# Kernel optimization log

Hardware: AMD Instinct MI355X
Metric: run time of the kernel (lower is better)

## Reference

```python
import jax, jax.numpy as jnp
import numpy as np

B, H, W = 4, 256, 256
IN_HSI, IN_MSI, EMBED = 31, 3, 128
R = 2
MAX_FLOW = 2.0
REG_IN = EMBED + EMBED + (2 * R + 1) ** 2 + 1  # 282


def _conv(x, w, b=None, pad=0, groups=1):
    out = jax.lax.conv_general_dilated(
        x, w, (1, 1), [(pad, pad), (pad, pad)],
        dimension_numbers=('NCHW', 'OIHW', 'NCHW'), feature_group_count=groups)
    if b is not None:
        out = out + b[None, :, None, None]
    return out


def _gauss_window(size=9, sigma=1.5):
    c = jnp.arange(size, dtype=jnp.float32) - (size - 1) / 2.0
    g = jnp.exp(-(c ** 2) / (2.0 * sigma ** 2))
    g = g / g.sum()
    return g[:, None] * g[None, :]


def _ssim_map(a, b, win=9):
    # standard gaussian-window SSIM, per-pixel map averaged over channels
    C = a.shape[1]
    w2d = _gauss_window(win)
    k = jnp.broadcast_to(w2d[None, None], (C, 1, win, win))
    pad = win // 2
    dw = lambda t: _conv(t, k, pad=pad, groups=C)
    mu1, mu2 = dw(a), dw(b)
    mu1s, mu2s, mu12 = mu1 * mu1, mu2 * mu2, mu1 * mu2
    s1 = dw(a * a) - mu1s
    s2 = dw(b * b) - mu2s
    s12 = dw(a * b) - mu12
    C1, C2 = 0.01 ** 2, 0.03 ** 2
    m = ((2 * mu12 + C1) * (2 * s12 + C2)) / ((mu1s + mu2s + C1) * (s1 + s2 + C2))
    return m.mean(axis=1)  # (B,H,W)


def _match_mean_std(src, ref, eps=1e-6):
    sm = src.mean(axis=(2, 3), keepdims=True)
    ss = src.std(axis=(2, 3), keepdims=True, ddof=1)  # torch std is unbiased
    rm = ref.mean(axis=(2, 3), keepdims=True)
    rs = ref.std(axis=(2, 3), keepdims=True, ddof=1)
    return (src - sm) / (ss + eps) * rs + rm


def _l2norm(t, eps=1e-12):
    n = jnp.sqrt(jnp.sum(t * t, axis=1, keepdims=True))
    return t / jnp.maximum(n, eps)


def _corr_volume(q, k, r=R):
    _, _, h, w = q.shape
    q = _l2norm(q)
    k = _l2norm(k)
    kp = jnp.pad(k, ((0, 0), (0, 0), (r, r), (r, r)), mode='edge')  # replicate pad
    outs = []
    for dy in range(-r, r + 1):
        for dx in range(-r, r + 1):
            ks = kp[:, :, r + dy:r + dy + h, r + dx:r + dx + w]
            outs.append(jnp.sum(q * ks, axis=1))
    return jnp.stack(outs, axis=1)  # (B, 25, H, W)


def _reflect(coord, size):
    # PyTorch grid_sample reflection, align_corners=False: reflect about -0.5 and size-0.5
    min_ = -0.5
    span = float(size)
    c = jnp.abs(coord - min_)
    extra = jnp.mod(c, span)
    flips = jnp.floor(c / span)
    c = jnp.where(jnp.mod(flips, 2.0) == 0.0, extra + min_, span - extra + min_)
    return jnp.clip(c, 0.0, size - 1.0)


def _warp(img, flow):
    b, c, h, w = img.shape
    gx = (-1.0 + (2.0 * jnp.arange(w, dtype=img.dtype) + 1.0) / w)[None, None, :] + flow[:, 0] * (2.0 / w)
    gy = (-1.0 + (2.0 * jnp.arange(h, dtype=img.dtype) + 1.0) / h)[None, :, None] + flow[:, 1] * (2.0 / h)
    ix = _reflect(((gx + 1.0) * w - 1.0) / 2.0, w)
    iy = _reflect(((gy + 1.0) * h - 1.0) / 2.0, h)
    x0 = jnp.floor(ix)
    y0 = jnp.floor(iy)
    wx = ix - x0
    wy = iy - y0
    x0i = jnp.clip(x0.astype(jnp.int32), 0, w - 1)
    x1i = jnp.clip(x0i + 1, 0, w - 1)
    y0i = jnp.clip(y0.astype(jnp.int32), 0, h - 1)
    y1i = jnp.clip(y0i + 1, 0, h - 1)
    bi = jnp.arange(b)[:, None, None]
    g = lambda yi, xi: img[bi, :, yi, xi]  # (B,H,W,C)
    out = (g(y0i, x0i) * ((1 - wy) * (1 - wx))[..., None]
           + g(y0i, x1i) * ((1 - wy) * wx)[..., None]
           + g(y1i, x0i) * (wy * (1 - wx))[..., None]
           + g(y1i, x1i) * (wy * wx)[..., None])
    return jnp.transpose(out, (0, 3, 1, 2))


def setup_inputs() -> dict:
    key = jax.random.key(0)
    ks = jax.random.split(key, 16)

    def rn(k, shape, fan_in):
        return (jax.random.normal(k, shape, dtype=jnp.float32) / np.sqrt(fan_in)).astype(jnp.float32)

    return {
        'x': jax.random.normal(ks[0], (B, 2 * IN_HSI, H, W), dtype=jnp.float32),
        'y': jax.random.normal(ks[1], (B, IN_MSI, H, W), dtype=jnp.float32),
        'SRF': jax.random.uniform(ks[2], (IN_MSI, IN_HSI), dtype=jnp.float32) / IN_HSI,
        'conv_half_w': rn(ks[3], (IN_HSI, 2 * IN_HSI, 1, 1), 2 * IN_HSI),
        'conv_half_b': jnp.zeros((IN_HSI,), jnp.float32),
        'q_w': rn(ks[4], (EMBED, IN_HSI, 1, 1), IN_HSI),
        'q_b': jnp.zeros((EMBED,), jnp.float32),
        'k_w': rn(ks[5], (EMBED, IN_MSI, 1, 1), IN_MSI),
        'k_b': jnp.zeros((EMBED,), jnp.float32),
        'r1_w': rn(ks[6], (128, REG_IN, 3, 3), REG_IN * 9),
        'r1_b': jnp.zeros((128,), jnp.float32),
        'r2_w': rn(ks[7], (64, 128, 3, 3), 128 * 9),
        'r2_b': jnp.zeros((64,), jnp.float32),
        'r3_w': rn(ks[8], (2, 64, 1, 1), 64) * 0.1,
        'r3_b': jnp.zeros((2,), jnp.float32),
    }


def reference(x, y, SRF, conv_half_w, conv_half_b, q_w, q_b, k_w, k_b,
              r1_w, r1_b, r2_w, r2_b, r3_w, r3_b):
    x = _conv(x, conv_half_w, conv_half_b)
    x_original = x
    srf_w = SRF[:, :, None, None]  # (in_msi, in_hsi, 1, 1)
    x_projected = jnp.clip(_conv(x, srf_w), -1.0, 1.0)
    x_aligned = jnp.clip(_match_mean_std(x_projected, y), -1.0, 1.0)
    ssim_score = _ssim_map(x_aligned, y, 9)
    difficulty = jnp.clip((1.0 - ssim_score)[:, None] / 2.0, 0.0, 1.0)  # (B,1,H,W)
    q = _conv(x, q_w, q_b)
    k = _conv(y, k_w, k_b)
    corr = _corr_volume(q, k, R)
    reg_in = jnp.concatenate([q, k, corr, difficulty], axis=1)
    h1 = jax.nn.leaky_relu(_conv(reg_in, r1_w, r1_b, pad=1), 0.2)
    h2 = jax.nn.leaky_relu(_conv(h1, r2_w, r2_b, pad=1), 0.2)
    flow = jnp.tanh(_conv(h2, r3_w, r3_b)) * MAX_FLOW * difficulty
    return _warp(x_original, flow)
```

## Files before the change

### kernel.cpp

```cpp
#include <hip/hip_runtime.h>
#include <hip/hip_bf16.h>
#include <math.h>


#define HH 256
#define WWI 256
#define HW 65536
#define CH 31
#define CIN2 62
#define CM 3
#define CE 128
#define REGC 288
#define C1S 1e-4f
#define C2S 9e-4f

typedef unsigned short u16;
typedef unsigned int u32;
typedef short bf16x8 __attribute__((ext_vector_type(8)));
typedef float f32x4 __attribute__((ext_vector_type(4)));

__device__ __forceinline__ float blo(u32 u){ return __uint_as_float(u << 16); }
__device__ __forceinline__ float bhi(u32 u){ return __uint_as_float(u & 0xffff0000u); }
__device__ __forceinline__ float b1f(u16 u){ return __uint_as_float(((u32)u) << 16); }
__device__ __forceinline__ u16 f2b(float f){
    u32 u = __float_as_uint(f);
    u32 r = (u + 0x7fffu + ((u >> 16) & 1u)) >> 16;
    return (u16)r;
}
__device__ __forceinline__ f32x4 mfma16(bf16x8 a, bf16x8 b, f32x4 c){
    return __builtin_amdgcn_mfma_f32_16x16x32_bf16(a, b, c, 0, 0, 0);
}

__global__ void k_conv_half(const float* __restrict__ x, const float* __restrict__ w,
                            const float* __restrict__ bias, u16* __restrict__ x31){
    __shared__ float sw[CH*CIN2];
    __shared__ float sb[CH+1];
    for(int i=threadIdx.x;i<CH*CIN2;i+=256) sw[i]=w[i];
    for(int i=threadIdx.x;i<CH;i+=256) sb[i]=bias[i];
    __syncthreads();
    int pixg = blockIdx.x*256 + threadIdx.x;
    int b = pixg>>16, hw = pixg&65535;
    float acc[CH];
    #pragma unroll
    for(int c=0;c<CH;c++) acc[c]=sb[c];
    for(int ci=0;ci<CIN2;ci++){
        float xv = x[((size_t)(b*CIN2+ci))*HW + hw];
        #pragma unroll
        for(int c=0;c<CH;c++) acc[c] += sw[c*CIN2+ci]*xv;
    }
    u16* o = x31 + (size_t)pixg*32;
    #pragma unroll
    for(int c=0;c<CH;c++) o[c]=f2b(acc[c]);
    o[31]=0;
}

__global__ void k_project(const u16* __restrict__ x31, const float* __restrict__ srf,
                          float* __restrict__ xp){
    __shared__ float s[CM*CH];
    for(int i=threadIdx.x;i<CM*CH;i+=256) s[i]=srf[i];
    __syncthreads();
    int pixg = blockIdx.x*256 + threadIdx.x;
    int b = pixg>>16, hw = pixg&65535;
    const u16* xr = x31 + (size_t)pixg*32;
    float xv[CH];
    #pragma unroll
    for(int c=0;c<CH;c++) xv[c] = b1f(xr[c]);
    #pragma unroll
    for(int m=0;m<CM;m++){
        float acc=0.f;
        #pragma unroll
        for(int c=0;c<CH;c++) acc += s[m*CH+c]*xv[c];
        acc = fminf(fmaxf(acc,-1.f),1.f);
        xp[((size_t)(b*CM+m))*HW + hw] = acc;
    }
}

__global__ void k_stats1(const float* __restrict__ xp, const float* __restrict__ y,
                         float2* __restrict__ part, int NB){
    int bid = blockIdx.x;
    int p = bid >> 6, c = bid & 63;
    const float* src = (p<3*NB) ? (xp + (size_t)p*HW) : (y + (size_t)(p-3*NB)*HW);
    const float4* s4 = (const float4*)(src + c*1024);
    float4 v = s4[threadIdx.x];
    float s  = v.x + v.y + v.z + v.w;
    float ss = v.x*v.x + v.y*v.y + v.z*v.z + v.w*v.w;
    #pragma unroll
    for(int t=1;t<64;t<<=1){ s += __shfl_xor(s,t); ss += __shfl_xor(ss,t); }
    __shared__ float rs[4], rss[4];
    int wid = threadIdx.x>>6, lane = threadIdx.x&63;
    if(lane==0){ rs[wid]=s; rss[wid]=ss; }
    __syncthreads();
    if(threadIdx.x==0){
        part[bid] = float2{rs[0]+rs[1]+rs[2]+rs[3], rss[0]+rss[1]+rss[2]+rss[3]};
    }
}

__global__ void k_stats2(const float2* __restrict__ part, float* __restrict__ stats){
    int p = blockIdx.x;
    float2 pa = part[p*64 + threadIdx.x];
    float s = pa.x, ss = pa.y;
    #pragma unroll
    for(int t=1;t<64;t<<=1){ s += __shfl_xor(s,t); ss += __shfl_xor(ss,t); }
    if(threadIdx.x==0){
        float mean = s/(float)HW;
        float var = (ss - s*s/(float)HW) / (float)(HW-1);
        stats[p*2]   = mean;
        stats[p*2+1] = sqrtf(fmaxf(var,0.f));
    }
}

__global__ __launch_bounds__(256) void k_ssim(const float* __restrict__ xp,
                                              const float* __restrict__ y,
                                              const float* __restrict__ stats,
                                              float* __restrict__ diff,
                                              u16* __restrict__ regin, int NB){
    __shared__ float sxa[1600];
    __shared__ float sy2[1600];
    __shared__ float hs[5][1280];
    int t = threadIdx.x;
    int bid = blockIdx.x;
    int bb = bid >> 6;
    int s2 = bid & 63;
    int tx = s2 & 7, ty = s2 >> 3;
    float g[9]; float gs = 0.f;
    #pragma unroll
    for(int k=0;k<9;k++){ float cc=(float)(k-4); g[k]=expf(-cc*cc/4.5f); gs+=g[k]; }
    float ginv = 1.f/gs;
    #pragma unroll
    for(int k=0;k<9;k++) g[k] *= ginv;

    float msum[4] = {0.f,0.f,0.f,0.f};
    for(int m=0;m<3;m++){
        int plane = bb*3+m;
        float sm = stats[plane*2],        ssd = stats[plane*2+1];
        float rm = stats[(plane+3*NB)*2], rsd = stats[(plane+3*NB)*2+1];
        const float* xpp = xp + (size_t)plane*HW;
        const float* yp  = y  + (size_t)plane*HW;
        if(m) __syncthreads();
        #pragma unroll
        for(int it=0; it<7; ++it){
            int s = it*256 + t;
            if(s < 1600){
                int rr = s/40, cc = s - rr*40;
                int gy = ty*32-4+rr, gx = tx*32-4+cc;
                float xv=0.f, yv=0.f;
                if(((unsigned)gy<256u)&&((unsigned)gx<256u)){
                    float v = xpp[(gy<<8)+gx];
                    v = (v-sm)/(ssd+1e-6f)*rsd + rm;
                    xv = fminf(fmaxf(v,-1.f),1.f);
                    yv = yp[(gy<<8)+gx];
                }
                sxa[s]=xv; sy2[s]=yv;
            }
        }
        __syncthreads();
        #pragma unroll
        for(int it=0; it<5; ++it){
            int s = it*256 + t;
            int rr = s>>5, cc = s&31;
            int base = rr*40 + cc;
            float s0=0,s1=0,s2v=0,s3=0,s4=0;
            #pragma unroll
            for(int k=0;k<9;k++){
                float gg=g[k];
                float a=sxa[base+k], b=sy2[base+k];
                s0+=gg*a; s1+=gg*b; s2v+=gg*a*a; s3+=gg*b*b; s4+=gg*a*b;
            }
            hs[0][s]=s0; hs[1][s]=s1; hs[2][s]=s2v; hs[3][s]=s3; hs[4][s]=s4;
        }
        __syncthreads();
        #pragma unroll
        for(int it=0; it<4; ++it){
            int s = it*256 + t;
            int rr = s>>5, cc = s&31;
            float v0=0,v1=0,v2=0,v3=0,v4=0;
            #pragma unroll
            for(int k=0;k<9;k++){
                float gg=g[k];
                int idx=(rr+k)*32+cc;
                v0+=gg*hs[0][idx]; v1+=gg*hs[1][idx]; v2+=gg*hs[2][idx];
                v3+=gg*hs[3][idx]; v4+=gg*hs[4][idx];
            }
            float mu1=v0, mu2=v1;
            float mu1s=mu1*mu1, mu2s=mu2*mu2, mu12=mu1*mu2;
            float sg1=v2-mu1s, sg2=v3-mu2s, sg12=v4-mu12;
            msum[it] += (2.f*mu12+C1S)*(2.f*sg12+C2S)
                      / ((mu1s+mu2s+C1S)*(sg1+sg2+C2S));
        }
    }
    #pragma unroll
    for(int it=0; it<4; ++it){
        int s = it*256 + t;
        int rr = s>>5, cc = s&31;
        int pixg = (bb<<16) + ((ty*32+rr)<<8) + (tx*32+cc);
        float d = fminf(fmaxf((1.f-msum[it]*(1.f/3.f))*0.5f,0.f),1.f);
        diff[pixg] = d;
        regin[(size_t)pixg*REGC + 281] = f2b(d);
    }
}

__global__ __launch_bounds__(128) void k_qk(const u16* __restrict__ x31,
                     const float* __restrict__ y,
                     const float* __restrict__ qw, const float* __restrict__ qb,
                     const float* __restrict__ kw, const float* __restrict__ kb,
                     u16* __restrict__ regin){
    __shared__ float sqw[CE*CH];
    __shared__ float skw[CE*CM];
    __shared__ float sqb[CE], skb[CE];
    for(int i=threadIdx.x;i<CE*CH;i+=128) sqw[i]=qw[i];
    for(int i=threadIdx.x;i<CE*CM;i+=128) skw[i]=kw[i];
    if(threadIdx.x<CE){ sqb[threadIdx.x]=qb[threadIdx.x]; skb[threadIdx.x]=kb[threadIdx.x]; }
    __syncthreads();
    int co = threadIdx.x;
    int p0 = blockIdx.x*32;
    float wk0 = skw[co*CM+0], wk1 = skw[co*CM+1], wk2 = skw[co*CM+2];
    for(int pp=0;pp<32;pp++){
        int pixg = p0+pp;
        int b = pixg>>16, hw = pixg&65535;
        const u16* xr = x31 + (size_t)pixg*32;
        float acc = sqb[co];
        #pragma unroll
        for(int c=0;c<CH;c++) acc += sqw[co*CH+c]*b1f(xr[c]);
        u16* rg = regin + (size_t)pixg*REGC;
        rg[co] = f2b(acc);
        float ack = skb[co] + wk0*y[((size_t)(b*CM  ))*HW+hw]
                            + wk1*y[((size_t)(b*CM+1))*HW+hw]
                            + wk2*y[((size_t)(b*CM+2))*HW+hw];
        rg[128+co] = f2b(ack);
        if(co<6) rg[282+co] = 0;
    }
}

__global__ __launch_bounds__(256) void k_corr(const u16* __restrict__ regin,
                                              u16* __restrict__ regout){
    __shared__ uint4 klv[288*16];
    __shared__ float kinvl[288];
    int t = threadIdx.x;
    int half = t & 1, pidx = t >> 1;
    int bid = blockIdx.x;
    int bb = bid >> 9;
    int s2 = bid & 511;
    int tx = s2 & 7, ty = s2 >> 3;
    int lw = pidx & 31, lh = pidx >> 5;
    int w = tx*32 + lw;
    int h = ty*4 + lh;
    int pixg = (bb<<16) + (h<<8) + w;

    #pragma unroll
    for(int it=0; it<18; ++it){
        int s = it*256 + t;
        int rpx = s >> 4, g = s & 15;
        int rr = rpx/36, cc = rpx - rr*36;
        int gy = min(max(ty*4-2+rr,0),255);
        int gx = min(max(tx*32-2+cc,0),255);
        const uint4* src = (const uint4*)(regin + ((size_t)((bb<<16)+(gy<<8)+gx))*REGC + 128);
        klv[rpx*16 + (g ^ (rpx&15))] = src[g];
    }
    __syncthreads();

    #pragma unroll
    for(int it=0; it<3; ++it){
        int item = it*256 + t;
        int px = item>>1, hf = item&1;
        float s = 0.f;
        if(item < 576){
            const uint4* kp = &klv[px*16];
            int sw = px & 15;
            #pragma unroll
            for(int i=0;i<8;i++){
                uint4 kv = kp[(hf*8+i)^sw];
                s += blo(kv.x)*blo(kv.x)+bhi(kv.x)*bhi(kv.x)
                   + blo(kv.y)*blo(kv.y)+bhi(kv.y)*bhi(kv.y)
                   + blo(kv.z)*blo(kv.z)+bhi(kv.z)*bhi(kv.z)
                   + blo(kv.w)*blo(kv.w)+bhi(kv.w)*bhi(kv.w);
            }
        }
        float so = s + __shfl_xor(s,1);
        if(item < 576 && hf==0) kinvl[px] = 1.f/fmaxf(sqrtf(so),1e-12f);
    }
    __syncthreads();

    uint4 q[8];
    const uint4* qp = (const uint4*)(regin + (size_t)pixg*REGC) + half*8;
    #pragma unroll
    for(int i=0;i<8;i++) q[i] = qp[i];
    float sq = 0.f;
    #pragma unroll
    for(int i=0;i<8;i++){
        uint4 v = q[i];
        sq += blo(v.x)*blo(v.x)+bhi(v.x)*bhi(v.x) + blo(v.y)*blo(v.y)+bhi(v.y)*bhi(v.y)
            + blo(v.z)*blo(v.z)+bhi(v.z)*bhi(v.z) + blo(v.w)*blo(v.w)+bhi(v.w)*bhi(v.w);
    }
    sq += __shfl_xor(sq, 1);
    float qn = 1.f/fmaxf(sqrtf(sq),1e-12f);

    float res[13];
    #pragma unroll
    for(int dy=-2;dy<=2;dy++){
        #pragma unroll
        for(int dx=-2;dx<=2;dx++){
            int rpx = (lh+2+dy)*36 + (lw+2+dx);
            const uint4* kp = &klv[rpx*16];
            int sw = rpx & 15;
            float s = 0.f;
            #pragma unroll
            for(int i=0;i<8;i++){
                uint4 kv = kp[(half*8 + i) ^ sw];
                uint4 qv = q[i];
                s += blo(qv.x)*blo(kv.x) + bhi(qv.x)*bhi(kv.x);
                s += blo(qv.y)*blo(kv.y) + bhi(qv.y)*bhi(kv.y);
                s += blo(qv.z)*blo(kv.z) + bhi(qv.z)*bhi(kv.z);
                s += blo(qv.w)*blo(kv.w) + bhi(qv.w)*bhi(kv.w);
            }
            s += __shfl_xor(s, 1);
            float cv = s*qn*kinvl[rpx];
            int o = (dy+2)*5 + (dx+2);
            if(o < 13){ if(half==0) res[o] = cv; }
            else      { if(half==1) res[o-13] = cv; }
        }
    }

    u16* rg = regout + (size_t)pixg*REGC + 256;
    if(half==0){
        u16 p[13];
        #pragma unroll
        for(int i=0;i<13;i++) p[i] = f2b(res[i]);
        uint4 v0; u32* v0p = (u32*)&v0;
        #pragma unroll
        for(int i=0;i<4;i++) v0p[i] = (u32)p[2*i] | ((u32)p[2*i+1]<<16);
        *(uint4*)(rg) = v0;
        *(u32*)(rg+8)  = (u32)p[8]  | ((u32)p[9]<<16);
        *(u32*)(rg+10) = (u32)p[10] | ((u32)p[11]<<16);
        rg[12] = p[12];
    } else {
        u16 p[12];
        #pragma unroll
        for(int i=0;i<12;i++) p[i] = f2b(res[i]);
        rg[13] = p[0];
        *(u32*)(rg+14) = (u32)p[1] | ((u32)p[2]<<16);
        uint4 v1; u32* v1p = (u32*)&v1;
        #pragma unroll
        for(int i=0;i<4;i++) v1p[i] = (u32)p[3+2*i] | ((u32)p[4+2*i]<<16);
        *(uint4*)(rg+16) = v1;
        rg[24] = p[11];
    }
}

__global__ void k_wre(const float* __restrict__ w1, const float* __restrict__ w2,
                      u16* __restrict__ w1f, u16* __restrict__ w2f,
                      u16* __restrict__ zpad){
    int i = blockIdx.x*256 + threadIdx.x;
    if(i < 32) zpad[i] = 0;
    if(i < 9*9*128*32){
        int j = i & 7;
        int gg = (i>>3)&3;
        int co = (i>>5)&127;
        int rest = i>>12;
        int kbg = rest%9, tap = rest/9;
        int ci = kbg*32 + gg*8 + j;
        float v = (ci<282) ? w1[((size_t)co*282 + ci)*9 + tap] : 0.f;
        w1f[i] = f2b(v);
    }
    if(i < 9*4*64*32){
        int j = i & 7;
        int gg = (i>>3)&3;
        int co = (i>>5)&63;
        int rest = i>>11;
        int kbg = rest&3, tap = rest>>2;
        int ci = kbg*32 + gg*8 + j;
        w2f[i] = f2b(w2[((size_t)co*128 + ci)*9 + tap]);
    }
}

template<int MF>
__device__ __forceinline__ void ldaM(const uint4* sbuf, int ky, int kx, int kb,
                                     int lane15, int lgrp, bf16x8* ar){
    #pragma unroll
    for(int mf=0;mf<MF;mf++){
        int spx  = (mf&1)*16 + lane15 + kx;
        int srow = (mf>>1) + ky;
        int slot = (srow*34 + spx)*8 + ((kb*4 + lgrp) ^ (spx&7));
        ar[mf] = *(const bf16x8*)&sbuf[slot];
    }
}

template<int NF, int KBGT, int NCO>
__device__ __forceinline__ void ldbN(const u16* __restrict__ wf, int kbg, int tap,
                                     int co0, int lane15, int lgrp, bf16x8* br){
    #pragma unroll
    for(int nf=0;nf<NF;nf++){
        size_t idx = ((size_t)((tap*KBGT + kbg)*NCO + co0 + nf*16 + lane15))*4 + lgrp;
        br[nf] = *(const bf16x8*)(wf + idx*8);
    }
}

template<int MF, int NF, int KBGT, int NCO, int KBI>
__device__ __forceinline__ void conv_steps(const uint4* sbuf, const u16* __restrict__ wf,
                                           int kbgbase, int co0, int lane15, int lgrp,
                                           f32x4 (&acc)[MF][NF]){
    constexpr int NST = 9*KBI;
    #pragma unroll
    for(int s=0;s<NST;s++){
        int ky,kx,kb;
        if(KBI==2){ ky = s/6; kx = (s>>1)%3; kb = s&1; }
        else      { ky = s/3; kx = s%3;      kb = 0;   }
        bf16x8 a[MF];
        bf16x8 b[NF];
        ldaM<MF>(sbuf, ky,kx,kb, lane15, lgrp, a);
        ldbN<NF,KBGT,NCO>(wf, kbgbase+kb, ky*3+kx, co0, lane15, lgrp, b);
        #pragma unroll
        for(int mf=0;mf<MF;mf++)
            #pragma unroll
            for(int nf=0;nf<NF;nf++)
                acc[mf][nf] = mfma16(a[mf], b[nf], acc[mf][nf]);
    }
}

template<int CSTRIDE, int CINTOT, int NCO, int KBGT, int TM>
__global__ __launch_bounds__(128, 1) void k_conv3(const u16* __restrict__ in,
                                                  const u16* __restrict__ wf,
                                                  const float* __restrict__ bias,
                                                  u16* __restrict__ out,
                                                  const u16* __restrict__ zpad){
    constexpr int NW = 2;
    constexpr int NF = NCO/(16*NW);
    constexpr int MF = 2*TM;
    constexpr int NCHUNK = (CINTOT + 63)/64;
    constexpr int NTH = NW*64;
    constexpr int SLOTS = (TM+2)*34*8;
    __shared__ uint4 sT[2*SLOTS];
    int t = threadIdx.x;
    int lane15 = t & 15, lgrp = (t >> 4) & 3;
    int co0 = (t >> 6) * (NCO/NW);
    int rb = blockIdx.x;
    int bid = (rb & 7)*(gridDim.x >> 3) + (rb >> 3);
    int bb = bid >> 9;
    int s2 = bid & 511;
    int tx = s2 & 7, ty = s2 >> 3;
    int row0 = ty*TM, col0 = tx*32;
    const u16* inb  = in  + (size_t)bb*HW*CSTRIDE;
    u16*       outb = out + (size_t)bb*HW*NCO;

    f32x4 acc[MF][NF];
    #pragma unroll
    for(int nf=0;nf<NF;nf++){
        float bsv = bias[co0 + nf*16 + lane15];
        #pragma unroll
        for(int mf=0;mf<MF;mf++) acc[mf][nf] = f32x4{bsv,bsv,bsv,bsv};
    }

    auto stage = [&](int buf, int kc){
        constexpr int NIT = (SLOTS + NTH - 1)/NTH;
        #pragma unroll
        for(int it=0; it<NIT; ++it){
            int s = it*NTH + t;
            if(s >= SLOTS) continue;
            int srow = s/272, rem = s - srow*272;
            int spx = rem>>3, ggp = rem&7;
            int gg = ggp ^ (spx&7);
            int gy = row0-1+srow, gx = col0-1+spx;
            bool ok = ((unsigned)gy<256u) && ((unsigned)gx<256u);
            const u16* src = ok ? (inb + (size_t)((gy<<8)+gx)*CSTRIDE + kc + gg*8) : zpad;
            __builtin_amdgcn_global_load_lds(
                (const __attribute__((address_space(1))) u32*)src,
                (__attribute__((address_space(3))) u32*)&sT[buf*SLOTS + s],
                16, 0, 0);
        }
    };

    stage(0, 0);
    __syncthreads();

    int cur = 0;
    for(int j=0;j<NCHUNK;j++){
        if(j+1 < NCHUNK) stage(cur^1, (j+1)*64);
        if(CINTOT==288 && j==NCHUNK-1)
            conv_steps<MF,NF,KBGT,NCO,1>(&sT[cur*SLOTS], wf, j*2, co0, lane15, lgrp, acc);
        else
            conv_steps<MF,NF,KBGT,NCO,2>(&sT[cur*SLOTS], wf, j*2, co0, lane15, lgrp, acc);
        if(j+1 < NCHUNK){
            __syncthreads();
            cur ^= 1;
        }
    }

    #pragma unroll
    for(int mf=0;mf<MF;mf++){
        int prow  = row0 + (mf>>1);
        int pcolb = col0 + (mf&1)*16 + lgrp*4;
        #pragma unroll
        for(int nf=0;nf<NF;nf++){
            int co = co0 + nf*16 + lane15;
            #pragma unroll
            for(int r=0;r<4;r++){
                int pix = (prow<<8) + pcolb + r;
                float v = acc[mf][nf][r];
                v = (v>0.f) ? v : 0.2f*v;
                outb[(size_t)pix*NCO + co] = f2b(v);
            }
        }
    }
}

__device__ __forceinline__ float reflectc(float coord, float size){
    float c = fabsf(coord + 0.5f);
    float extra = fmodf(c, size);
    float flips = floorf(c/size);
    float fo = fmodf(flips, 2.0f);
    float r = (fo == 0.0f) ? (extra - 0.5f) : (size - extra - 0.5f);
    return fminf(fmaxf(r, 0.0f), size - 1.0f);
}

__global__ void k_flowwarp(const u16* __restrict__ h2, const float* __restrict__ w3,
                           const float* __restrict__ b3, const float* __restrict__ diff,
                           const u16* __restrict__ x31, float* __restrict__ out){
    __shared__ float sw[130];
    for(int i=threadIdx.x;i<128;i+=256) sw[i]=w3[i];
    if(threadIdx.x<2) sw[128+threadIdx.x]=b3[threadIdx.x];
    __syncthreads();
    int pixg = blockIdx.x*256 + threadIdx.x;
    int b = pixg>>16, hw = pixg&65535, h = hw>>8, w = hw&255;
    const uint4* h4 = (const uint4*)(h2 + (size_t)pixg*64);
    float f0 = sw[128], f1 = sw[129];
    #pragma unroll
    for(int cc=0;cc<8;cc++){
        uint4 u = h4[cc];
        float vv[8] = {blo(u.x),bhi(u.x),blo(u.y),bhi(u.y),blo(u.z),bhi(u.z),blo(u.w),bhi(u.w)};
        #pragma unroll
        for(int j=0;j<8;j++){ int c = cc*8+j; f0 += sw[c]*vv[j]; f1 += sw[64+c]*vv[j]; }
    }
    float d = diff[pixg];
    f0 = tanhf(f0)*2.0f*d;
    f1 = tanhf(f1)*2.0f*d;
    float ix = reflectc((float)w + f0, 256.f);
    float iy = reflectc((float)h + f1, 256.f);
    float x0 = floorf(ix), y0 = floorf(iy);
    float wx = ix-x0, wy = iy-y0;
    int x0i = min(max((int)x0,0),255);
    int x1i = min(x0i+1,255);
    int y0i = min(max((int)y0,0),255);
    int y1i = min(y0i+1,255);
    const u16* p00 = x31 + ((size_t)((b<<16)+(y0i<<8)+x0i))*32;
    const u16* p01 = x31 + ((size_t)((b<<16)+(y0i<<8)+x1i))*32;
    const u16* p10 = x31 + ((size_t)((b<<16)+(y1i<<8)+x0i))*32;
    const u16* p11 = x31 + ((size_t)((b<<16)+(y1i<<8)+x1i))*32;
    float w00=(1.f-wy)*(1.f-wx), w01=(1.f-wy)*wx, w10=wy*(1.f-wx), w11=wy*wx;
    float* ob = out + (size_t)b*CH*HW + hw;
    #pragma unroll
    for(int c=0;c<CH;c++){
        ob[(size_t)c*HW] = w00*b1f(p00[c]) + w01*b1f(p01[c])
                         + w10*b1f(p10[c]) + w11*b1f(p11[c]);
    }
}

extern "C" void kernel_launch(void* const* d_in, const int* in_sizes, int n_in,
                              void* d_out, int out_size, void* d_ws, size_t ws_size,
                              hipStream_t stream) {
    const float* x    = (const float*)d_in[0];
    const float* y    = (const float*)d_in[1];
    const float* srf  = (const float*)d_in[2];
    const float* chw  = (const float*)d_in[3];
    const float* chb  = (const float*)d_in[4];
    const float* qw   = (const float*)d_in[5];
    const float* qb   = (const float*)d_in[6];
    const float* kw   = (const float*)d_in[7];
    const float* kb   = (const float*)d_in[8];
    const float* w1   = (const float*)d_in[9];
    const float* b1p  = (const float*)d_in[10];
    const float* w2   = (const float*)d_in[11];
    const float* b2p  = (const float*)d_in[12];
    const float* w3   = (const float*)d_in[13];
    const float* b3p  = (const float*)d_in[14];

    struct Arena {
        u16 *x31, *regin, *h1, *h2, *w1f, *w2f, *zpad;
        float *xp, *stats, *diff;
        float2 *part;
    };
    auto layout = [&](char* base, int G, Arena* A)->size_t{
        size_t o = 0;
        auto take = [&](size_t sz)->char*{ char* p = base ? base+o : 0; o += (sz+255)&~255ull; return p; };
        Arena tmpA; Arena* P = A ? A : &tmpA;
        P->x31   = (u16*)  take((size_t)G*HW*32*2);
        P->xp    = (float*)take((size_t)G*3*HW*4);
        P->stats = (float*)take(6*4*2*4);
        P->part  = (float2*)take((size_t)6*4*64*8);
        P->diff  = (float*)take((size_t)G*HW*4);
        P->regin = (u16*)  take((size_t)G*HW*REGC*2);
        P->h1    = (u16*)  take((size_t)G*HW*128*2);
        P->h2    = (u16*)  take((size_t)G*HW*64*2);
        P->w1f   = (u16*)  take((size_t)9*9*128*32*2);
        P->w2f   = (u16*)  take((size_t)9*4*64*32*2);
        P->zpad  = (u16*)  take(64);
        return o;
    };

    int G = 4;
    while(G > 1 && layout(nullptr, G, nullptr) > ws_size) G >>= 1;
    Arena A;
    layout((char*)d_ws, G, &A);

    k_wre<<<1296, 256, 0, stream>>>(w1, w2, A.w1f, A.w2f, A.zpad);

    for(int g0=0; g0<4; g0+=G){
        int NB = G;
        const float* xg  = x + (size_t)g0*CIN2*HW;
        const float* yg  = y + (size_t)g0*CM*HW;
        float* outg      = (float*)d_out + (size_t)g0*CH*HW;

        k_conv_half<<<NB*256,  256, 0, stream>>>(xg, chw, chb, A.x31);
        k_project  <<<NB*256,  256, 0, stream>>>(A.x31, srf, A.xp);
        k_stats1   <<<NB*384,  256, 0, stream>>>(A.xp, yg, A.part, NB);
        k_stats2   <<<NB*6,     64, 0, stream>>>(A.part, A.stats);
        k_ssim     <<<NB*64,   256, 0, stream>>>(A.xp, yg, A.stats, A.diff, A.regin, NB);
        k_qk       <<<NB*2048, 128, 0, stream>>>(A.x31, yg, qw, qb, kw, kb, A.regin);
        k_corr     <<<NB*512,  256, 0, stream>>>(A.regin, A.regin);
        k_conv3<288,288,128,9,4><<<NB*512, 128, 0, stream>>>(A.regin, A.w1f, b1p, A.h1, A.zpad);
        k_conv3<128,128, 64,4,4><<<NB*512, 128, 0, stream>>>(A.h1, A.w2f, b2p, A.h2, A.zpad);
        k_flowwarp <<<NB*256,  256, 0, stream>>>(A.h2, w3, b3p, A.diff, A.x31, outg);
    }
}
```

Baseline: 720.0 us.

## Fuse SRF projection into conv_half and halve corr LDS footprint via two passes

```diff
diff --git a/kernel.cpp b/kernel.cpp
--- a/kernel.cpp
+++ b/kernel.cpp
@@ -32,11 +32,14 @@
 }
 
 __global__ void k_conv_half(const float* __restrict__ x, const float* __restrict__ w,
-                            const float* __restrict__ bias, u16* __restrict__ x31){
+                            const float* __restrict__ bias, const float* __restrict__ srf,
+                            u16* __restrict__ x31, float* __restrict__ xp){
     __shared__ float sw[CH*CIN2];
     __shared__ float sb[CH+1];
+    __shared__ float ssrf[CM*CH];
     for(int i=threadIdx.x;i<CH*CIN2;i+=256) sw[i]=w[i];
     for(int i=threadIdx.x;i<CH;i+=256) sb[i]=bias[i];
+    for(int i=threadIdx.x;i<CM*CH;i+=256) ssrf[i]=srf[i];
     __syncthreads();
     int pixg = blockIdx.x*256 + threadIdx.x;
     int b = pixg>>16, hw = pixg&65535;
@@ -52,26 +55,13 @@
     #pragma unroll
     for(int c=0;c<CH;c++) o[c]=f2b(acc[c]);
     o[31]=0;
-}
-
-__global__ void k_project(const u16* __restrict__ x31, const float* __restrict__ srf,
-                          float* __restrict__ xp){
-    __shared__ float s[CM*CH];
-    for(int i=threadIdx.x;i<CM*CH;i+=256) s[i]=srf[i];
-    __syncthreads();
-    int pixg = blockIdx.x*256 + threadIdx.x;
-    int b = pixg>>16, hw = pixg&65535;
-    const u16* xr = x31 + (size_t)pixg*32;
-    float xv[CH];
-    #pragma unroll
-    for(int c=0;c<CH;c++) xv[c] = b1f(xr[c]);
     #pragma unroll
     for(int m=0;m<CM;m++){
-        float acc=0.f;
-        #pragma unroll
-        for(int c=0;c<CH;c++) acc += s[m*CH+c]*xv[c];
-        acc = fminf(fmaxf(acc,-1.f),1.f);
-        xp[((size_t)(b*CM+m))*HW + hw] = acc;
+        float a=0.f;
+        #pragma unroll
+        for(int c=0;c<CH;c++) a += ssrf[m*CH+c]*acc[c];
+        a = fminf(fmaxf(a,-1.f),1.f);
+        xp[((size_t)(b*CM+m))*HW + hw] = a;
     }
 }
 
@@ -231,9 +221,9 @@
     }
 }
 
-__global__ __launch_bounds__(256) void k_corr(const u16* __restrict__ regin,
-                                              u16* __restrict__ regout){
-    __shared__ uint4 klv[288*16];
+__global__ __launch_bounds__(256, 4) void k_corr(const u16* __restrict__ regin,
+                                                 u16* __restrict__ regout){
+    __shared__ uint4 klv[288*8];
     __shared__ float kinvl[288];
     int t = threadIdx.x;
     int half = t & 1, pidx = t >> 1;
@@ -246,85 +236,102 @@
     int h = ty*4 + lh;
     int pixg = (bb<<16) + (h<<8) + w;
 
-    #pragma unroll
-    for(int it=0; it<18; ++it){
-        int s = it*256 + t;
-        int rpx = s >> 4, g = s & 15;
-        int rr = rpx/36, cc = rpx - rr*36;
-        int gy = min(max(ty*4-2+rr,0),255);
-        int gx = min(max(tx*32-2+cc,0),255);
-        const uint4* src = (const uint4*)(regin + ((size_t)((bb<<16)+(gy<<8)+gx))*REGC + 128);
-        klv[rpx*16 + (g ^ (rpx&15))] = src[g];
-    }
-    __syncthreads();
+    const uint4* qbase = (const uint4*)(regin + (size_t)pixg*REGC);
+    uint4 q0[4], q1[4];
+    #pragma unroll
+    for(int i=0;i<4;i++){ q0[i] = qbase[half*4 + i]; q1[i] = qbase[8 + half*4 + i]; }
+    float sq = 0.f;
+    #pragma unroll
+    for(int i=0;i<4;i++){
+        uint4 a = q0[i], b = q1[i];
+        sq += blo(a.x)*blo(a.x)+bhi(a.x)*bhi(a.x) + blo(a.y)*blo(a.y)+bhi(a.y)*bhi(a.y)
+            + blo(a.z)*blo(a.z)+bhi(a.z)*bhi(a.z) + blo(a.w)*blo(a.w)+bhi(a.w)*bhi(a.w);
+        sq += blo(b.x)*blo(b.x)+bhi(b.x)*bhi(b.x) + blo(b.y)*blo(b.y)+bhi(b.y)*bhi(b.y)
+            + blo(b.z)*blo(b.z)+bhi(b.z)*bhi(b.z) + blo(b.w)*blo(b.w)+bhi(b.w)*bhi(b.w);
+    }
+    sq += __shfl_xor(sq, 1);
+    float qn = 1.f/fmaxf(sqrtf(sq),1e-12f);
+
+    float res[13];
+    #pragma unroll
+    for(int i=0;i<13;i++) res[i]=0.f;
+    float ksum[3] = {0.f,0.f,0.f};
+
+    #pragma unroll
+    for(int pass=0; pass<2; ++pass){
+        if(pass) __syncthreads();
+        #pragma unroll
+        for(int it=0; it<9; ++it){
+            int s = it*256 + t;
+            int rpx = s >> 3, g = s & 7;
+            int rr = rpx/36, cc = rpx - rr*36;
+            int gy = min(max(ty*4-2+rr,0),255);
+            int gx = min(max(tx*32-2+cc,0),255);
+            const uint4* src = (const uint4*)(regin + ((size_t)((bb<<16)+(gy<<8)+gx))*REGC + 128)
+                             + pass*8;
+            klv[rpx*8 + (g ^ (rpx&7))] = src[g];
+        }
+        __syncthreads();
+        #pragma unroll
+        for(int it=0; it<3; ++it){
+            int item = it*256 + t;
+            if(item < 576){
+                int px = item>>1, hf = item&1;
+                const uint4* kp = &klv[px*8];
+                int sw = px & 7;
+                float s = 0.f;
+                #pragma unroll
+                for(int i=0;i<4;i++){
+                    uint4 kv = kp[(hf*4+i)^sw];
+                    s += blo(kv.x)*blo(kv.x)+bhi(kv.x)*bhi(kv.x)
+                       + blo(kv.y)*blo(kv.y)+bhi(kv.y)*bhi(kv.y)
+                       + blo(kv.z)*blo(kv.z)+bhi(kv.z)*bhi(kv.z)
+                       + blo(kv.w)*blo(kv.w)+bhi(kv.w)*bhi(kv.w);
+                }
+                ksum[it] += s;
+            }
+        }
+        #pragma unroll
+        for(int dy=-2;dy<=2;dy++){
+            #pragma unroll
+            for(int dx=-2;dx<=2;dx++){
+                int rpx = (lh+2+dy)*36 + (lw+2+dx);
+                const uint4* kp = &klv[rpx*8];
+                int sw = rpx & 7;
+                float s = 0.f;
+                #pragma unroll
+                for(int i=0;i<4;i++){
+                    uint4 kv = kp[(half*4 + i) ^ sw];
+                    uint4 qv = pass ? q1[i] : q0[i];
+                    s += blo(qv.x)*blo(kv.x) + bhi(qv.x)*bhi(kv.x);
+                    s += blo(qv.y)*blo(kv.y) + bhi(qv.y)*bhi(kv.y);
+                    s += blo(qv.z)*blo(kv.z) + bhi(qv.z)*bhi(kv.z);
+                    s += blo(qv.w)*blo(kv.w) + bhi(qv.w)*bhi(kv.w);
+                }
+                s += __shfl_xor(s, 1);
+                int o = (dy+2)*5 + (dx+2);
+                if(o < 13){ if(half==0) res[o] += s; }
+                else      { if(half==1) res[o-13] += s; }
+            }
+        }
+    }
 
     #pragma unroll
     for(int it=0; it<3; ++it){
         int item = it*256 + t;
-        int px = item>>1, hf = item&1;
-        float s = 0.f;
-        if(item < 576){
-            const uint4* kp = &klv[px*16];
-            int sw = px & 15;
-            #pragma unroll
-            for(int i=0;i<8;i++){
-                uint4 kv = kp[(hf*8+i)^sw];
-                s += blo(kv.x)*blo(kv.x)+bhi(kv.x)*bhi(kv.x)
-                   + blo(kv.y)*blo(kv.y)+bhi(kv.y)*bhi(kv.y)
-                   + blo(kv.z)*blo(kv.z)+bhi(kv.z)*bhi(kv.z)
-                   + blo(kv.w)*blo(kv.w)+bhi(kv.w)*bhi(kv.w);
-            }
-        }
-        float so = s + __shfl_xor(s,1);
-        if(item < 576 && hf==0) kinvl[px] = 1.f/fmaxf(sqrtf(so),1e-12f);
+        float so = ksum[it] + __shfl_xor(ksum[it],1);
+        if(item < 576 && (item&1)==0) kinvl[item>>1] = 1.f/fmaxf(sqrtf(so),1e-12f);
     }
     __syncthreads();
-
-    uint4 q[8];
-    const uint4* qp = (const uint4*)(regin + (size_t)pixg*REGC) + half*8;
-    #pragma unroll
-    for(int i=0;i<8;i++) q[i] = qp[i];
-    float sq = 0.f;
-    #pragma unroll
-    for(int i=0;i<8;i++){
-        uint4 v = q[i];
-        sq += blo(v.x)*blo(v.x)+bhi(v.x)*bhi(v.x) + blo(v.y)*blo(v.y)+bhi(v.y)*bhi(v.y)
-            + blo(v.z)*blo(v.z)+bhi(v.z)*bhi(v.z) + blo(v.w)*blo(v.w)+bhi(v.w)*bhi(v.w);
-    }
-    sq += __shfl_xor(sq, 1);
-    float qn = 1.f/fmaxf(sqrtf(sq),1e-12f);
-
-    float res[13];
-    #pragma unroll
-    for(int dy=-2;dy<=2;dy++){
-        #pragma unroll
-        for(int dx=-2;dx<=2;dx++){
-            int rpx = (lh+2+dy)*36 + (lw+2+dx);
-            const uint4* kp = &klv[rpx*16];
-            int sw = rpx & 15;
-            float s = 0.f;
-            #pragma unroll
-            for(int i=0;i<8;i++){
-                uint4 kv = kp[(half*8 + i) ^ sw];
-                uint4 qv = q[i];
-                s += blo(qv.x)*blo(kv.x) + bhi(qv.x)*bhi(kv.x);
-                s += blo(qv.y)*blo(kv.y) + bhi(qv.y)*bhi(kv.y);
-                s += blo(qv.z)*blo(kv.z) + bhi(qv.z)*bhi(kv.z);
-                s += blo(qv.w)*blo(kv.w) + bhi(qv.w)*bhi(kv.w);
-            }
-            s += __shfl_xor(s, 1);
-            float cv = s*qn*kinvl[rpx];
-            int o = (dy+2)*5 + (dx+2);
-            if(o < 13){ if(half==0) res[o] = cv; }
-            else      { if(half==1) res[o-13] = cv; }
-        }
-    }
 
     u16* rg = regout + (size_t)pixg*REGC + 256;
     if(half==0){
         u16 p[13];
         #pragma unroll
-        for(int i=0;i<13;i++) p[i] = f2b(res[i]);
+        for(int i=0;i<13;i++){
+            int rpx = (lh+2+(i/5-2))*36 + (lw+2+(i%5-2));
+            p[i] = f2b(res[i]*qn*kinvl[rpx]);
+        }
         uint4 v0; u32* v0p = (u32*)&v0;
         #pragma unroll
         for(int i=0;i<4;i++) v0p[i] = (u32)p[2*i] | ((u32)p[2*i+1]<<16);
@@ -335,7 +342,11 @@
     } else {
         u16 p[12];
         #pragma unroll
-        for(int i=0;i<12;i++) p[i] = f2b(res[i]);
+        for(int i=0;i<12;i++){
+            int o = 13+i;
+            int rpx = (lh+2+(o/5-2))*36 + (lw+2+(o%5-2));
+            p[i] = f2b(res[i]*qn*kinvl[rpx]);
+        }
         rg[13] = p[0];
         *(u32*)(rg+14) = (u32)p[1] | ((u32)p[2]<<16);
         uint4 v1; u32* v1p = (u32*)&v1;
@@ -608,8 +619,7 @@
         const float* yg  = y + (size_t)g0*CM*HW;
         float* outg      = (float*)d_out + (size_t)g0*CH*HW;
 
-        k_conv_half<<<NB*256,  256, 0, stream>>>(xg, chw, chb, A.x31);
-        k_project  <<<NB*256,  256, 0, stream>>>(A.x31, srf, A.xp);
+        k_conv_half<<<NB*256,  256, 0, stream>>>(xg, chw, chb, srf, A.x31, A.xp);
         k_stats1   <<<NB*384,  256, 0, stream>>>(A.xp, yg, A.part, NB);
         k_stats2   <<<NB*6,     64, 0, stream>>>(A.part, A.stats);
         k_ssim     <<<NB*64,   256, 0, stream>>>(A.xp, yg, A.stats, A.diff, A.regin, NB);
```

After: 857.2 us. 1.19x slower.
